# Kernel optimization log

Measured on AMD Instinct MI355X. Metric: run time of the kernel, lower is better.

## Reference

```python
import jax, jax.numpy as jnp
import numpy as np

BN_EPS = 1e-5


def setup_inputs() -> dict:
    key = jax.random.key(0)
    ks = jax.random.split(key, 5)
    B, N, M, C = 2, 8192, 8192, 3
    return {
        "x": jax.random.normal(ks[0], (B, N, C), dtype=jnp.float32),
        "y": jax.random.normal(ks[1], (B, M, C), dtype=jnp.float32),
        "W1": jax.random.normal(ks[2], (256, 20), dtype=jnp.float32) * 0.1,
        "gamma1": jnp.ones((256,), jnp.float32),
        "beta1": jnp.zeros((256,), jnp.float32),
        "mean1": jnp.zeros((256,), jnp.float32),
        "var1": jnp.ones((256,), jnp.float32),
        "W2": jax.random.normal(ks[3], (128, 256), dtype=jnp.float32) * 0.1,
        "gamma2": jnp.ones((128,), jnp.float32),
        "beta2": jnp.zeros((128,), jnp.float32),
        "mean2": jnp.zeros((128,), jnp.float32),
        "var2": jnp.ones((128,), jnp.float32),
        "W3": jax.random.normal(ks[4], (1, 128), dtype=jnp.float32) * 0.1,
        "k": 20,
    }


def _bn(x, gamma, beta, mean, var):
    # x: [B, C, N]; inference-mode BatchNorm1d
    inv = gamma * jax.lax.rsqrt(var + BN_EPS)
    return x * inv[None, :, None] + (beta - mean * inv)[None, :, None]


def reference(x, y, W1, gamma1, beta1, mean1, var1,
              W2, gamma2, beta2, mean2, var2, W3, k):
    # x: [B,N,C], y: [B,M,C]
    xx = jnp.sum(x * x, axis=-1)                      # [B,N]
    yy = jnp.sum(y * y, axis=-1)                      # [B,M]
    inner = jnp.einsum('bnc,bmc->bnm', x, y)          # [B,N,M]
    # negative squared pairwise distance (as in torch code)
    pd = 2.0 * inner - xx[:, :, None] - yy[:, None, :]
    dist, _ = jax.lax.top_k(pd, k)                    # [B,N,k], descending = k nearest
    feat = jnp.transpose(dist, (0, 2, 1))             # [B,k,N]
    h = jax.nn.relu(_bn(jnp.einsum('oc,bcn->bon', W1, feat), gamma1, beta1, mean1, var1))
    h = jax.nn.relu(_bn(jnp.einsum('oc,bcn->bon', W2, h), gamma2, beta2, mean2, var2))
    out = jax.nn.sigmoid(jnp.einsum('oc,bcn->bon', W3, h))  # [B,1,N]
    return jnp.transpose(out, (0, 2, 1))              # [B,N,1]
```

## Files before the change

### kernel.cpp

```cpp
#include <hip/hip_runtime.h>
#include <hip/hip_bf16.h>
#include <math.h>


#define M_CAND 8192
#define NROWS 16384
#define KSEL 20
#define MPL 4
#define RPW 4
#define TPAIRS 256
#define NTILES 16

typedef float v2f __attribute__((ext_vector_type(2)));

__device__ __forceinline__ float med3f(float a, float b, float c) {
    return __builtin_amdgcn_fmed3f(a, b, c);
}

__device__ __forceinline__ v2f fma2(v2f a, v2f b, v2f c) {
#if __has_builtin(__builtin_elementwise_fma)
    return __builtin_elementwise_fma(a, b, c);
#else
    v2f r; r.x = fmaf(a.x, b.x, c.x); r.y = fmaf(a.y, b.y, c.y); return r;
#endif
}

__global__ __launch_bounds__(256) void k_prep(const float* __restrict__ y,
                                              const float* __restrict__ w2,
                                              float4* __restrict__ ysp,
                                              float* __restrict__ w2t) {
    int idx = blockIdx.x * 256 + threadIdx.x;
    if (idx < 8192) {
        int b = idx >> 12, q = idx & 4095;
        const float* p0 = y + (size_t)(b * M_CAND + 2 * q) * 3;
        float a0 = p0[0], a1 = p0[1], a2 = p0[2];
        float b0 = p0[3], b1 = p0[4], b2 = p0[5];
        float nwa = -(a0 * a0 + a1 * a1 + a2 * a2);
        float nwb = -(b0 * b0 + b1 * b1 + b2 * b2);
        float4* base = ysp + b * 8192;
        base[q]        = make_float4(a0, b0, a1, b1);
        base[4096 + q] = make_float4(a2, b2, nwa, nwb);
    } else {
        int j = idx - 8192;
        int o = j >> 8, kk = j & 255;
        w2t[kk * 128 + o] = w2[j];
    }
}

__global__ __launch_bounds__(256, 4) void k_knn(const float* __restrict__ x,
                                                const float4* __restrict__ ysp,
                                                float* __restrict__ dfeat) {
    __shared__ float4 tileA[TPAIRS];
    __shared__ float4 tileB[TPAIRS];
    const int tid  = threadIdx.x;
    const int wid  = tid >> 6;
    const int lane = tid & 63;
    const int qbase = (blockIdx.x * 4 + wid) * RPW;
    const int b = qbase >> 13;

    float tx0[RPW], tx1[RPW], tx2[RPW], xxn[RPW];
#pragma unroll
    for (int r = 0; r < RPW; ++r) {
        float a0 = x[(qbase + r) * 3 + 0];
        float a1 = x[(qbase + r) * 3 + 1];
        float a2 = x[(qbase + r) * 3 + 2];
        tx0[r] = 2.0f * a0; tx1[r] = 2.0f * a1; tx2[r] = 2.0f * a2;
        xxn[r] = -(a0 * a0 + a1 * a1 + a2 * a2);
    }
    const float4* ybA = ysp + b * 8192;
    const float4* ybB = ybA + 4096;

    float bl[RPW][MPL];
#pragma unroll
    for (int r = 0; r < RPW; ++r)
#pragma unroll
        for (int j = 0; j < MPL; ++j) bl[r][j] = -3.0e38f;

#define PROCESS_PAIR(Aq, Bq)                                                   \
    {                                                                          \
        v2f y0p = {(Aq).x, (Aq).y};                                            \
        v2f y1p = {(Aq).z, (Aq).w};                                            \
        v2f y2p = {(Bq).x, (Bq).y};                                            \
        v2f nwp = {(Bq).z, (Bq).w};                                            \
        _Pragma("unroll")                                                      \
        for (int r = 0; r < RPW; ++r) {                                        \
            v2f t0 = {tx0[r], tx0[r]};                                         \
            v2f t1 = {tx1[r], tx1[r]};                                         \
            v2f t2 = {tx2[r], tx2[r]};                                         \
            v2f xp = {xxn[r], xxn[r]};                                         \
            v2f pd = fma2(t0, y0p, fma2(t1, y1p, fma2(t2, y2p, xp))) + nwp;    \
            float va = pd.x, vb = pd.y;                                        \
            bl[r][3] = med3f(va, bl[r][2], bl[r][3]);                          \
            bl[r][2] = med3f(va, bl[r][1], bl[r][2]);                          \
            bl[r][1] = med3f(va, bl[r][0], bl[r][1]);                          \
            bl[r][0] = fmaxf(bl[r][0], va);                                    \
            bl[r][3] = med3f(vb, bl[r][2], bl[r][3]);                          \
            bl[r][2] = med3f(vb, bl[r][1], bl[r][2]);                          \
            bl[r][1] = med3f(vb, bl[r][0], bl[r][1]);                          \
            bl[r][0] = fmaxf(bl[r][0], vb);                                    \
        }                                                                      \
    }

    float4 rA = ybA[tid], rB = ybB[tid];
#pragma unroll 1
    for (int t = 0; t < NTILES; ++t) {
        tileA[tid] = rA;
        tileB[tid] = rB;
        __syncthreads();
        if (t + 1 < NTILES) {
            rA = ybA[(t + 1) * TPAIRS + tid];
            rB = ybB[(t + 1) * TPAIRS + tid];
        }
        const float4* tA = tileA + lane;
        const float4* tB = tileB + lane;
#pragma unroll
        for (int j = 0; j < 4; ++j) {
            float4 A = tA[j * 64];
            float4 Bv = tB[j * 64];
            PROCESS_PAIR(A, Bv)
        }
        __syncthreads();
    }

    unsigned needmask = 0;
#pragma unroll
    for (int q = 0; q < RPW; ++q) {
        float h0 = bl[q][0], h1 = bl[q][1], h2 = bl[q][2], h3 = bl[q][3];
        int pops = 0;
        float sel = 0.0f;
        for (int r = 0; r < KSEL; ++r) {
            float mx = h0;
#pragma unroll
            for (int off = 32; off >= 1; off >>= 1) mx = fmaxf(mx, __shfl_xor(mx, off, 64));
            unsigned long long ball = __ballot(h0 == mx);
            int winner = (int)__ffsll(ball) - 1;
            bool win = (lane == winner);
            h0 = win ? h1 : h0;
            h1 = win ? h2 : h1;
            h2 = win ? h3 : h2;
            h3 = win ? -3.0e38f : h3;
            pops += win ? 1 : 0;
            if (lane == r) sel = mx;
        }
        if (__ballot(pops >= MPL) != 0ULL) needmask |= (1u << q);
        if (lane < KSEL) dfeat[(size_t)(qbase + q) * KSEL + lane] = sel;
    }

    if (needmask != 0) {
#pragma unroll
        for (int q = 0; q < RPW; ++q) {
            if (!(needmask & (1u << q))) continue;
            float a[KSEL];
#pragma unroll
            for (int j = 0; j < KSEL; ++j) a[j] = -3.0e38f;
#pragma unroll 1
            for (int t = 0; t < 32; ++t) {
                float4 dA0 = ybA[t * 128 + lane], dA1 = ybA[t * 128 + 64 + lane];
                float4 dB0 = ybB[t * 128 + lane], dB1 = ybB[t * 128 + 64 + lane];
                v2f t0 = {tx0[q], tx0[q]};
                v2f t1 = {tx1[q], tx1[q]};
                v2f t2 = {tx2[q], tx2[q]};
                v2f xp = {xxn[q], xxn[q]};
                v2f pd0 = fma2(t0, (v2f){dA0.x, dA0.y},
                          fma2(t1, (v2f){dA0.z, dA0.w},
                          fma2(t2, (v2f){dB0.x, dB0.y}, xp))) + (v2f){dB0.z, dB0.w};
                v2f pd1 = fma2(t0, (v2f){dA1.x, dA1.y},
                          fma2(t1, (v2f){dA1.z, dA1.w},
                          fma2(t2, (v2f){dB1.x, dB1.y}, xp))) + (v2f){dB1.z, dB1.w};
                float vv[4] = {pd0.x, pd0.y, pd1.x, pd1.y};
#pragma unroll
                for (int i = 0; i < 4; ++i) {
                    float v = vv[i];
#pragma unroll
                    for (int jj = KSEL - 1; jj >= 1; --jj) a[jj] = med3f(v, a[jj - 1], a[jj]);
                    a[0] = fmaxf(a[0], v);
                }
            }
            float sel2 = 0.0f;
            for (int r = 0; r < KSEL; ++r) {
                float mx = a[0];
#pragma unroll
                for (int off = 32; off >= 1; off >>= 1) mx = fmaxf(mx, __shfl_xor(mx, off, 64));
                unsigned long long ball = __ballot(a[0] == mx);
                int winner = (int)__ffsll(ball) - 1;
                bool win = (lane == winner);
#pragma unroll
                for (int jj = 0; jj < KSEL - 1; ++jj) a[jj] = win ? a[jj + 1] : a[jj];
                a[KSEL - 1] = win ? -3.0e38f : a[KSEL - 1];
                if (lane == r) sel2 = mx;
            }
            if (lane < KSEL) dfeat[(size_t)(qbase + q) * KSEL + lane] = sel2;
        }
    }
#undef PROCESS_PAIR
}

__global__ __launch_bounds__(256) void k_mlp(const float* __restrict__ dfeat,
                                             const float* __restrict__ W1,
                                             const float* __restrict__ g1,
                                             const float* __restrict__ be1,
                                             const float* __restrict__ mu1,
                                             const float* __restrict__ va1,
                                             const float* __restrict__ W2T,
                                             const float* __restrict__ g2,
                                             const float* __restrict__ be2,
                                             const float* __restrict__ mu2,
                                             const float* __restrict__ va2,
                                             const float* __restrict__ W3,
                                             float* __restrict__ out) {
    __shared__ float h1l[32 * 260];
    const int t = threadIdx.x;
    const int rowbase = blockIdx.x * 32;

    float w[KSEL];
#pragma unroll
    for (int j = 0; j < KSEL; j += 4) {
        float4 q = *(const float4*)(W1 + t * KSEL + j);
        w[j] = q.x; w[j + 1] = q.y; w[j + 2] = q.z; w[j + 3] = q.w;
    }
    const float s1  = g1[t] * rsqrtf(va1[t] + 1e-5f);
    const float bc1 = be1[t] - mu1[t] * s1;

    for (int r = 0; r < 32; ++r) {
        const float* dr = dfeat + (size_t)(rowbase + r) * KSEL;
        float dv[KSEL];
#pragma unroll
        for (int j = 0; j < KSEL; j += 4) {
            float4 q = *(const float4*)(dr + j);
            dv[j] = q.x; dv[j + 1] = q.y; dv[j + 2] = q.z; dv[j + 3] = q.w;
        }
        float acc0 = 0.f, acc1 = 0.f;
#pragma unroll
        for (int j = 0; j < KSEL; j += 2) {
            acc0 = fmaf(w[j], dv[j], acc0);
            acc1 = fmaf(w[j + 1], dv[j + 1], acc1);
        }
        h1l[r * 260 + t] = fmaxf(0.f, fmaf(s1, acc0 + acc1, bc1));
    }
    __syncthreads();

    const int og = t & 15;
    const int rq = t >> 4;
    float acc[2][8];
#pragma unroll
    for (int r = 0; r < 2; ++r)
#pragma unroll
        for (int i = 0; i < 8; ++i) acc[r][i] = 0.f;

    for (int kq = 0; kq < 64; ++kq) {
        const int k = kq * 4;
        float4 hq[2];
#pragma unroll
        for (int rr = 0; rr < 2; ++rr)
            hq[rr] = *(const float4*)(&h1l[(rq * 2 + rr) * 260 + k]);
        float4 wq[8];
#pragma unroll
        for (int kk = 0; kk < 4; ++kk) {
            wq[kk]     = *(const float4*)(W2T + (k + kk) * 128 + og * 4);
            wq[4 + kk] = *(const float4*)(W2T + (k + kk) * 128 + 64 + og * 4);
        }
#pragma unroll
        for (int r = 0; r < 2; ++r) {
            const float* hh = (const float*)&hq[r];
#pragma unroll
            for (int kk = 0; kk < 4; ++kk) {
                const float hval = hh[kk];
                const float* w0 = (const float*)&wq[kk];
                const float* w1 = (const float*)&wq[4 + kk];
#pragma unroll
                for (int i = 0; i < 4; ++i) {
                    acc[r][i]     = fmaf(hval, w0[i], acc[r][i]);
                    acc[r][4 + i] = fmaf(hval, w1[i], acc[r][4 + i]);
                }
            }
        }
    }

    float s2v[8], b2v[8], w3v[8];
#pragma unroll
    for (int h = 0; h < 2; ++h)
#pragma unroll
        for (int i = 0; i < 4; ++i) {
            const int o = h * 64 + og * 4 + i;
            const float sv = g2[o] * rsqrtf(va2[o] + 1e-5f);
            s2v[h * 4 + i] = sv;
            b2v[h * 4 + i] = be2[o] - mu2[o] * sv;
            w3v[h * 4 + i] = W3[o];
        }
#pragma unroll
    for (int r = 0; r < 2; ++r) {
        float c = 0.f;
#pragma unroll
        for (int i = 0; i < 8; ++i) {
            float h2 = fmaxf(0.f, fmaf(s2v[i], acc[r][i], b2v[i]));
            c = fmaf(w3v[i], h2, c);
        }
#pragma unroll
        for (int off = 8; off >= 1; off >>= 1) c += __shfl_xor(c, off, 64);
        if (og == 0) {
            out[rowbase + rq * 2 + r] = 1.0f / (1.0f + expf(-c));
        }
    }
}

extern "C" void kernel_launch(void* const* d_in, const int* in_sizes, int n_in,
                              void* d_out, int out_size, void* d_ws, size_t ws_size,
                              hipStream_t stream) {
    const float* x   = (const float*)d_in[0];
    const float* y   = (const float*)d_in[1];
    const float* W1  = (const float*)d_in[2];
    const float* g1  = (const float*)d_in[3];
    const float* be1 = (const float*)d_in[4];
    const float* mu1 = (const float*)d_in[5];
    const float* va1 = (const float*)d_in[6];
    const float* W2  = (const float*)d_in[7];
    const float* g2  = (const float*)d_in[8];
    const float* be2 = (const float*)d_in[9];
    const float* mu2 = (const float*)d_in[10];
    const float* va2 = (const float*)d_in[11];
    const float* W3  = (const float*)d_in[12];
    float* out = (float*)d_out;

    char* ws = (char*)d_ws;
    float4* ysp  = (float4*)(ws);
    float* dfeat = (float*)(ws + 262144);
    float* w2t   = (float*)(ws + 262144 + 1310720);

    k_prep<<<160, 256, 0, stream>>>(y, W2, ysp, w2t);
    k_knn <<<1024, 256, 0, stream>>>(x, ysp, dfeat);
    k_mlp <<<512, 256, 0, stream>>>(dfeat, W1, g1, be1, mu1, va1,
                                    w2t, g2, be2, mu2, va2, W3, out);
}
```

Measured before the change: 127.0 us.

## Split KNN candidate scan across two waves and merge partial top-k lists

Each group of four query rows is now scanned by two wavefronts, each covering half of the candidate set, and the two per-row top-20 lists are merged through shared memory with a shuffle-based merge-path max/min step. The candidate data layout becomes structure-of-arrays (x, y, z, negated norm planes) read directly from global memory, which removes the shared-memory tile staging and its per-tile barriers. The grid doubles and occupancy hints rise to 8 blocks per CU, giving more waves to hide latency. In exchange every lane reads candidates straight from global or L2, and the kernel gains a merge step plus a barrier.

```diff
diff --git a/kernel.cpp b/kernel.cpp
--- a/kernel.cpp
+++ b/kernel.cpp
@@ -8,8 +8,6 @@
 #define KSEL 20
 #define MPL 4
 #define RPW 4
-#define TPAIRS 256
-#define NTILES 16
 
 typedef float v2f __attribute__((ext_vector_type(2)));
 
@@ -27,35 +25,35 @@
 
 __global__ __launch_bounds__(256) void k_prep(const float* __restrict__ y,
                                               const float* __restrict__ w2,
-                                              float4* __restrict__ ysp,
+                                              float* __restrict__ ys,
                                               float* __restrict__ w2t) {
     int idx = blockIdx.x * 256 + threadIdx.x;
-    if (idx < 8192) {
-        int b = idx >> 12, q = idx & 4095;
-        const float* p0 = y + (size_t)(b * M_CAND + 2 * q) * 3;
-        float a0 = p0[0], a1 = p0[1], a2 = p0[2];
-        float b0 = p0[3], b1 = p0[4], b2 = p0[5];
-        float nwa = -(a0 * a0 + a1 * a1 + a2 * a2);
-        float nwb = -(b0 * b0 + b1 * b1 + b2 * b2);
-        float4* base = ysp + b * 8192;
-        base[q]        = make_float4(a0, b0, a1, b1);
-        base[4096 + q] = make_float4(a2, b2, nwa, nwb);
+    if (idx < NROWS) {
+        int b = idx >> 13, m = idx & 8191;
+        const float* p = y + (size_t)idx * 3;
+        float y0 = p[0], y1 = p[1], y2 = p[2];
+        float* base = ys + (size_t)b * 4 * M_CAND + m;
+        base[0]          = y0;
+        base[M_CAND]     = y1;
+        base[2 * M_CAND] = y2;
+        base[3 * M_CAND] = -(y0 * y0 + y1 * y1 + y2 * y2);
     } else {
-        int j = idx - 8192;
+        int j = idx - NROWS;
         int o = j >> 8, kk = j & 255;
         w2t[kk * 128 + o] = w2[j];
     }
 }
 
-__global__ __launch_bounds__(256, 4) void k_knn(const float* __restrict__ x,
-                                                const float4* __restrict__ ysp,
+__global__ __launch_bounds__(256, 8) void k_knn(const float* __restrict__ x,
+                                                const float* __restrict__ ys,
                                                 float* __restrict__ dfeat) {
-    __shared__ float4 tileA[TPAIRS];
-    __shared__ float4 tileB[TPAIRS];
+    __shared__ float mxbuf[2][RPW][2][KSEL];
     const int tid  = threadIdx.x;
     const int wid  = tid >> 6;
     const int lane = tid & 63;
-    const int qbase = (blockIdx.x * 4 + wid) * RPW;
+    const int g    = wid >> 1;
+    const int h    = wid & 1;
+    const int qbase = blockIdx.x * 8 + g * 4;
     const int b = qbase >> 13;
 
     float tx0[RPW], tx1[RPW], tx2[RPW], xxn[RPW];
@@ -67,8 +65,11 @@
         tx0[r] = 2.0f * a0; tx1[r] = 2.0f * a1; tx2[r] = 2.0f * a2;
         xxn[r] = -(a0 * a0 + a1 * a1 + a2 * a2);
     }
-    const float4* ybA = ysp + b * 8192;
-    const float4* ybB = ybA + 4096;
+    const float4* q0 = (const float4*)(ys + (size_t)(b * 4 + 0) * M_CAND);
+    const float4* q1 = (const float4*)(ys + (size_t)(b * 4 + 1) * M_CAND);
+    const float4* q2 = (const float4*)(ys + (size_t)(b * 4 + 2) * M_CAND);
+    const float4* q3 = (const float4*)(ys + (size_t)(b * 4 + 3) * M_CAND);
+    const int hbase = h * 1024;
 
     float bl[RPW][MPL];
 #pragma unroll
@@ -76,52 +77,43 @@
 #pragma unroll
         for (int j = 0; j < MPL; ++j) bl[r][j] = -3.0e38f;
 
-#define PROCESS_PAIR(Aq, Bq)                                                   \
-    {                                                                          \
-        v2f y0p = {(Aq).x, (Aq).y};                                            \
-        v2f y1p = {(Aq).z, (Aq).w};                                            \
-        v2f y2p = {(Bq).x, (Bq).y};                                            \
-        v2f nwp = {(Bq).z, (Bq).w};                                            \
-        _Pragma("unroll")                                                      \
-        for (int r = 0; r < RPW; ++r) {                                        \
-            v2f t0 = {tx0[r], tx0[r]};                                         \
-            v2f t1 = {tx1[r], tx1[r]};                                         \
-            v2f t2 = {tx2[r], tx2[r]};                                         \
-            v2f xp = {xxn[r], xxn[r]};                                         \
-            v2f pd = fma2(t0, y0p, fma2(t1, y1p, fma2(t2, y2p, xp))) + nwp;    \
-            float va = pd.x, vb = pd.y;                                        \
-            bl[r][3] = med3f(va, bl[r][2], bl[r][3]);                          \
-            bl[r][2] = med3f(va, bl[r][1], bl[r][2]);                          \
-            bl[r][1] = med3f(va, bl[r][0], bl[r][1]);                          \
-            bl[r][0] = fmaxf(bl[r][0], va);                                    \
-            bl[r][3] = med3f(vb, bl[r][2], bl[r][3]);                          \
-            bl[r][2] = med3f(vb, bl[r][1], bl[r][2]);                          \
-            bl[r][1] = med3f(vb, bl[r][0], bl[r][1]);                          \
-            bl[r][0] = fmaxf(bl[r][0], vb);                                    \
-        }                                                                      \
-    }
-
-    float4 rA = ybA[tid], rB = ybB[tid];
 #pragma unroll 1
-    for (int t = 0; t < NTILES; ++t) {
-        tileA[tid] = rA;
-        tileB[tid] = rB;
-        __syncthreads();
-        if (t + 1 < NTILES) {
-            rA = ybA[(t + 1) * TPAIRS + tid];
-            rB = ybB[(t + 1) * TPAIRS + tid];
-        }
-        const float4* tA = tileA + lane;
-        const float4* tB = tileB + lane;
-#pragma unroll
-        for (int j = 0; j < 4; ++j) {
-            float4 A = tA[j * 64];
-            float4 Bv = tB[j * 64];
-            PROCESS_PAIR(A, Bv)
-        }
-        __syncthreads();
-    }
-
+    for (int t = 0; t < 16; ++t) {
+        const int idx = hbase + t * 64 + lane;
+        float4 A0 = q0[idx], A1 = q1[idx], A2 = q2[idx], A3 = q3[idx];
+        v2f y0a = {A0.x, A0.y}, y0b = {A0.z, A0.w};
+        v2f y1a = {A1.x, A1.y}, y1b = {A1.z, A1.w};
+        v2f y2a = {A2.x, A2.y}, y2b = {A2.z, A2.w};
+        v2f nwa = {A3.x, A3.y}, nwb = {A3.z, A3.w};
+#pragma unroll
+        for (int r = 0; r < RPW; ++r) {
+            v2f t0 = {tx0[r], tx0[r]};
+            v2f t1 = {tx1[r], tx1[r]};
+            v2f t2 = {tx2[r], tx2[r]};
+            v2f xp = {xxn[r], xxn[r]};
+            v2f pa = fma2(t0, y0a, fma2(t1, y1a, fma2(t2, y2a, xp))) + nwa;
+            v2f pb = fma2(t0, y0b, fma2(t1, y1b, fma2(t2, y2b, xp))) + nwb;
+            float v0 = pa.x, v1 = pa.y, v2v = pb.x, v3 = pb.y;
+            bl[r][3] = med3f(v0, bl[r][2], bl[r][3]);
+            bl[r][2] = med3f(v0, bl[r][1], bl[r][2]);
+            bl[r][1] = med3f(v0, bl[r][0], bl[r][1]);
+            bl[r][0] = fmaxf(bl[r][0], v0);
+            bl[r][3] = med3f(v1, bl[r][2], bl[r][3]);
+            bl[r][2] = med3f(v1, bl[r][1], bl[r][2]);
+            bl[r][1] = med3f(v1, bl[r][0], bl[r][1]);
+            bl[r][0] = fmaxf(bl[r][0], v1);
+            bl[r][3] = med3f(v2v, bl[r][2], bl[r][3]);
+            bl[r][2] = med3f(v2v, bl[r][1], bl[r][2]);
+            bl[r][1] = med3f(v2v, bl[r][0], bl[r][1]);
+            bl[r][0] = fmaxf(bl[r][0], v2v);
+            bl[r][3] = med3f(v3, bl[r][2], bl[r][3]);
+            bl[r][2] = med3f(v3, bl[r][1], bl[r][2]);
+            bl[r][1] = med3f(v3, bl[r][0], bl[r][1]);
+            bl[r][0] = fmaxf(bl[r][0], v3);
+        }
+    }
+
+    float selv[RPW];
     unsigned needmask = 0;
 #pragma unroll
     for (int q = 0; q < RPW; ++q) {
@@ -143,7 +135,7 @@
             if (lane == r) sel = mx;
         }
         if (__ballot(pops >= MPL) != 0ULL) needmask |= (1u << q);
-        if (lane < KSEL) dfeat[(size_t)(qbase + q) * KSEL + lane] = sel;
+        selv[q] = sel;
     }
 
     if (needmask != 0) {
@@ -154,23 +146,17 @@
 #pragma unroll
             for (int j = 0; j < KSEL; ++j) a[j] = -3.0e38f;
 #pragma unroll 1
-            for (int t = 0; t < 32; ++t) {
-                float4 dA0 = ybA[t * 128 + lane], dA1 = ybA[t * 128 + 64 + lane];
-                float4 dB0 = ybB[t * 128 + lane], dB1 = ybB[t * 128 + 64 + lane];
-                v2f t0 = {tx0[q], tx0[q]};
-                v2f t1 = {tx1[q], tx1[q]};
-                v2f t2 = {tx2[q], tx2[q]};
-                v2f xp = {xxn[q], xxn[q]};
-                v2f pd0 = fma2(t0, (v2f){dA0.x, dA0.y},
-                          fma2(t1, (v2f){dA0.z, dA0.w},
-                          fma2(t2, (v2f){dB0.x, dB0.y}, xp))) + (v2f){dB0.z, dB0.w};
-                v2f pd1 = fma2(t0, (v2f){dA1.x, dA1.y},
-                          fma2(t1, (v2f){dA1.z, dA1.w},
-                          fma2(t2, (v2f){dB1.x, dB1.y}, xp))) + (v2f){dB1.z, dB1.w};
-                float vv[4] = {pd0.x, pd0.y, pd1.x, pd1.y};
+            for (int t = 0; t < 16; ++t) {
+                const int idx = hbase + t * 64 + lane;
+                float4 A0 = q0[idx], A1 = q1[idx], A2 = q2[idx], A3 = q3[idx];
+                const float* e0 = (const float*)&A0;
+                const float* e1 = (const float*)&A1;
+                const float* e2 = (const float*)&A2;
+                const float* e3 = (const float*)&A3;
 #pragma unroll
                 for (int i = 0; i < 4; ++i) {
-                    float v = vv[i];
+                    float v = fmaf(tx0[q], e0[i], fmaf(tx1[q], e1[i],
+                              fmaf(tx2[q], e2[i], xxn[q]))) + e3[i];
 #pragma unroll
                     for (int jj = KSEL - 1; jj >= 1; --jj) a[jj] = med3f(v, a[jj - 1], a[jj]);
                     a[0] = fmaxf(a[0], v);
@@ -189,10 +175,30 @@
                 a[KSEL - 1] = win ? -3.0e38f : a[KSEL - 1];
                 if (lane == r) sel2 = mx;
             }
-            if (lane < KSEL) dfeat[(size_t)(qbase + q) * KSEL + lane] = sel2;
-        }
-    }
-#undef PROCESS_PAIR
+            selv[q] = sel2;
+        }
+    }
+
+#pragma unroll
+    for (int q = 0; q < RPW; ++q)
+        if (lane < KSEL) mxbuf[g][q][h][lane] = selv[q];
+    __syncthreads();
+
+#pragma unroll
+    for (int qq = 0; qq < 2; ++qq) {
+        const int q = h * 2 + qq;
+        float vA = (lane < KSEL) ? mxbuf[g][q][0][lane] : -3.0e38f;
+        float vB = (lane < KSEL) ? mxbuf[g][q][1][lane] : -3.0e38f;
+        float m = fmaxf(vA, vB);
+#pragma unroll
+        for (int j = 0; j < KSEL - 1; ++j) {
+            float aj = __shfl(vA, j, 64);
+            float bj = __shfl(vB, (lane - 1 - j) & 63, 64);
+            float t = fminf(aj, bj);
+            m = (j < lane) ? fmaxf(m, t) : m;
+        }
+        if (lane < KSEL) dfeat[(size_t)(qbase + q) * KSEL + lane] = m;
+    }
 }
 
 __global__ __launch_bounds__(256) void k_mlp(const float* __restrict__ dfeat,
@@ -278,14 +284,14 @@
 
     float s2v[8], b2v[8], w3v[8];
 #pragma unroll
-    for (int h = 0; h < 2; ++h)
+    for (int hh = 0; hh < 2; ++hh)
 #pragma unroll
         for (int i = 0; i < 4; ++i) {
-            const int o = h * 64 + og * 4 + i;
+            const int o = hh * 64 + og * 4 + i;
             const float sv = g2[o] * rsqrtf(va2[o] + 1e-5f);
-            s2v[h * 4 + i] = sv;
-            b2v[h * 4 + i] = be2[o] - mu2[o] * sv;
-            w3v[h * 4 + i] = W3[o];
+            s2v[hh * 4 + i] = sv;
+            b2v[hh * 4 + i] = be2[o] - mu2[o] * sv;
+            w3v[hh * 4 + i] = W3[o];
         }
 #pragma unroll
     for (int r = 0; r < 2; ++r) {
@@ -322,12 +328,12 @@
     float* out = (float*)d_out;
 
     char* ws = (char*)d_ws;
-    float4* ysp  = (float4*)(ws);
+    float* ys    = (float*)(ws);
     float* dfeat = (float*)(ws + 262144);
     float* w2t   = (float*)(ws + 262144 + 1310720);
 
-    k_prep<<<160, 256, 0, stream>>>(y, W2, ysp, w2t);
-    k_knn <<<1024, 256, 0, stream>>>(x, ysp, dfeat);
+    k_prep<<<192, 256, 0, stream>>>(y, W2, ys, w2t);
+    k_knn <<<2048, 256, 0, stream>>>(x, ys, dfeat);
     k_mlp <<<512, 256, 0, stream>>>(dfeat, W1, g1, be1, mu1, va1,
                                     w2t, g2, be2, mu2, va2, W3, out);
 }
```

Result: slower. 182.8 us (+43.9%).
